# Kernel tuning notes

Hardware: AMD Instinct MI355X
Metric: run time of the kernel (lower is better)

Reference implementation:

```python
import jax, jax.numpy as jnp
import numpy as np

B, H, LQ, LKV, D = 2, 4, 512, 512, 64


def setup_inputs() -> dict:
    key = jax.random.key(0)
    ks = jax.random.split(key, 6)
    queries = jax.random.normal(ks[0], (B, H, LQ, D), dtype=jnp.float32)
    keys = jax.random.normal(ks[1], (B, H, LKV, D), dtype=jnp.float32)
    values = jax.random.normal(ks[2], (B, H, LKV, D), dtype=jnp.float32)
    mask = jax.random.randint(ks[3], (B, LQ, LKV), 0, 2) > 0  # bool [B, Lq, Lkv]
    # linear_concat: weight [D, 2D] (normal std=0.02), bias zeros
    W_concat = jax.random.normal(ks[4], (D, 2 * D), dtype=jnp.float32) * 0.02
    b_concat = jnp.zeros((D,), dtype=jnp.float32)
    # linear_logit: weight [1, D] -> vector [D], bias scalar zero
    w_logit = jax.random.normal(ks[5], (D,), dtype=jnp.float32) * 0.02
    b_logit = jnp.zeros((), dtype=jnp.float32)
    return dict(queries=queries, keys=keys, values=values, mask=mask,
                W_concat=W_concat, b_concat=b_concat,
                w_logit=w_logit, b_logit=b_logit)


def reference(queries, keys, values, mask, W_concat, b_concat, w_logit, b_logit):
    d = queries.shape[-1]
    # cat(q, k) @ W.T == q @ W[:, :d].T + k @ W[:, d:].T  (exact split of the concat-linear)
    qp = jnp.einsum('bhqd,ed->bhqe', queries, W_concat[:, :d])   # [B,H,Lq,D]
    kp = jnp.einsum('bhkd,ed->bhke', keys, W_concat[:, d:])      # [B,H,Lkv,D]
    combined = jnp.tanh(qp[:, :, :, None, :] + kp[:, :, None, :, :] + b_concat)  # [B,H,Lq,Lkv,D]
    logits = jnp.einsum('bhqke,e->bhqk', combined, w_logit) + b_logit            # [B,H,Lq,Lkv]
    # mask handling: invert; rows fully masked get un-masked (avoid all -inf softmax)
    inv = ~mask  # [B,Lq,Lkv]
    inv = jnp.where(jnp.all(inv, axis=-1, keepdims=True), False, inv)
    inv = inv[:, None, :, :]  # broadcast over heads
    logits = jnp.where(inv, -jnp.inf, logits)
    weights = jax.nn.softmax(logits, axis=-1)
    if weights.shape[1] == 1:  # torch .squeeze(dim=1) semantics
        weights = jnp.squeeze(weights, axis=1)
    return weights
```

## Files before the change

### kernel.cpp

```cpp
#include <hip/hip_runtime.h>
#include <hip/hip_bf16.h>


#define NQROWS 4096

__global__ __launch_bounds__(256) void proj_kernel(
    const float* __restrict__ Q, const float* __restrict__ K,
    const float* __restrict__ W, const float* __restrict__ bC,
    float* __restrict__ eq, float* __restrict__ ekt)
{
  const int t  = threadIdx.x;
  const int tr = t >> 6;
  const int e  = t & 63;
  const int rbase = blockIdx.x * 8;
  const bool isK = rbase >= NQROWS;
  const int r0 = isK ? rbase - NQROWS : rbase;
  const float* __restrict__ src = isK ? K : Q;
  const int off = isK ? 64 : 0;

  __shared__ float  srow[8][64];
  __shared__ float4 wsh[64][16];
  __shared__ float  trsp[64][9];

  for (int i = t; i < 8 * 64; i += 256)
    srow[i >> 6][i & 63] = src[(r0 + (i >> 6)) * 64 + (i & 63)];
  for (int i = t; i < 64 * 16; i += 256) {
    const int er = i >> 4, d4 = i & 15;
    wsh[er][d4 ^ (er & 7)] =
        reinterpret_cast<const float4*>(W + er * 128 + off)[d4];
  }
  __syncthreads();

  float acc0 = 0.f, acc1 = 0.f;
  const int rA = tr * 2;
  #pragma unroll
  for (int d4 = 0; d4 < 16; ++d4) {
    const float4 w4 = wsh[e][d4 ^ (e & 7)];
    const float4 s0 = *reinterpret_cast<const float4*>(&srow[rA + 0][d4 * 4]);
    const float4 s1 = *reinterpret_cast<const float4*>(&srow[rA + 1][d4 * 4]);
    acc0 = fmaf(s0.x, w4.x, acc0); acc0 = fmaf(s0.y, w4.y, acc0);
    acc0 = fmaf(s0.z, w4.z, acc0); acc0 = fmaf(s0.w, w4.w, acc0);
    acc1 = fmaf(s1.x, w4.x, acc1); acc1 = fmaf(s1.y, w4.y, acc1);
    acc1 = fmaf(s1.z, w4.z, acc1); acc1 = fmaf(s1.w, w4.w, acc1);
  }

  const float C2 = 2.8853900817779268f;
  if (!isK) {
    const float bias = bC[e];
    eq[(r0 + rA + 0) * 64 + e] = __builtin_amdgcn_exp2f((acc0 + bias) * C2);
    eq[(r0 + rA + 1) * 64 + e] = __builtin_amdgcn_exp2f((acc1 + bias) * C2);
  } else {
    trsp[e][rA + 0] = __builtin_amdgcn_exp2f(acc0 * C2);
    trsp[e][rA + 1] = __builtin_amdgcn_exp2f(acc1 * C2);
    __syncthreads();
    const int bh = r0 >> 9;
    const int k0 = r0 & 511;
    float* __restrict__ dst = ekt + bh * 64 * 512 + k0;
    #pragma unroll
    for (int iter = 0; iter < 2; ++iter) {
      const int i  = t + iter * 256;
      const int e2 = i >> 3, kk = i & 7;
      dst[e2 * 512 + kk] = trsp[e2][kk];
    }
  }
}

__global__ __launch_bounds__(256) void attn_kernel(
    const float* __restrict__ eq, const float* __restrict__ ekt,
    const float* __restrict__ wl, const int* __restrict__ mask,
    float* __restrict__ out)
{
  const int t  = threadIdx.x;
  const int g  = t >> 7;
  const int c  = t & 127;
  const int wv = t >> 6;
  const int ln = t & 63;
  const int bh = blockIdx.x & 7;
  const int qg = blockIdx.x >> 3;
  const int b  = bh >> 2;
  const int q0 = qg * 4;
  const int r0 = q0 + g * 2;

  __shared__ float qsh[4][64];
  __shared__ float w2s[64];
  __shared__ float s_sm[4][2], s_sr[4][2];
  __shared__ int   s_any[4][2];

  if (t < 64) w2s[t] = -2.0f * wl[t];
  qsh[t >> 6][t & 63] = eq[(bh * 512 + q0 + (t >> 6)) * 64 + (t & 63)];
  __syncthreads();

  const float4* __restrict__ kq =
      reinterpret_cast<const float4*>(ekt + bh * 64 * 512) + c;

  float4 a0 = {0.f, 0.f, 0.f, 0.f};
  float4 a1 = {0.f, 0.f, 0.f, 0.f};

#define QUADC(AC, QV, C)                                                      \
  {                                                                           \
    const float t0 = fmaf(QV.x, K0.C, 1.f);                                   \
    const float t1 = fmaf(QV.y, K1.C, 1.f);                                   \
    const float t2 = fmaf(QV.z, K2.C, 1.f);                                   \
    const float t3 = fmaf(QV.w, K3.C, 1.f);                                   \
    const float t01 = t0 * t1, t23 = t2 * t3;                                 \
    const float den = t01 * t23;                                              \
    const float n01 = fmaf(w4.x, t1, w4.y * t0);                              \
    const float n23 = fmaf(w4.z, t3, w4.w * t2);                              \
    const float num = fmaf(n01, t23, n23 * t01);                              \
    AC.C = fmaf(num, __builtin_amdgcn_rcpf(den), AC.C);                       \
  }
#define QROW(AC, QV) QUADC(AC, QV, x) QUADC(AC, QV, y) \
                     QUADC(AC, QV, z) QUADC(AC, QV, w)

  #pragma unroll 4
  for (int eb = 0; eb < 16; ++eb) {
    const float4 K0 = kq[(eb * 4 + 0) * 128];
    const float4 K1 = kq[(eb * 4 + 1) * 128];
    const float4 K2 = kq[(eb * 4 + 2) * 128];
    const float4 K3 = kq[(eb * 4 + 3) * 128];
    const float4 qa = *reinterpret_cast<const float4*>(&qsh[g * 2 + 0][eb * 4]);
    const float4 qb = *reinterpret_cast<const float4*>(&qsh[g * 2 + 1][eb * 4]);
    const float4 w4 = *reinterpret_cast<const float4*>(&w2s[eb * 4]);
    QROW(a0, qa) QROW(a1, qb)
  }

  const int* __restrict__ mb = mask + (b * 512 + r0) * 512 + 4 * c;
  const int4 mv0 = *reinterpret_cast<const int4*>(mb);
  const int4 mv1 = *reinterpret_cast<const int4*>(mb + 512);

  const float L2E = 1.4426950408889634f;
  float4 p0, p1;
  p0.x = __builtin_amdgcn_exp2f(a0.x * L2E);
  p0.y = __builtin_amdgcn_exp2f(a0.y * L2E);
  p0.z = __builtin_amdgcn_exp2f(a0.z * L2E);
  p0.w = __builtin_amdgcn_exp2f(a0.w * L2E);
  p1.x = __builtin_amdgcn_exp2f(a1.x * L2E);
  p1.y = __builtin_amdgcn_exp2f(a1.y * L2E);
  p1.z = __builtin_amdgcn_exp2f(a1.z * L2E);
  p1.w = __builtin_amdgcn_exp2f(a1.w * L2E);

  float sm0 = ((mv0.x ? p0.x : 0.f) + (mv0.y ? p0.y : 0.f)) +
              ((mv0.z ? p0.z : 0.f) + (mv0.w ? p0.w : 0.f));
  float sm1 = ((mv1.x ? p1.x : 0.f) + (mv1.y ? p1.y : 0.f)) +
              ((mv1.z ? p1.z : 0.f) + (mv1.w ? p1.w : 0.f));
  float sr0 = (p0.x + p0.y) + (p0.z + p0.w);
  float sr1 = (p1.x + p1.y) + (p1.z + p1.w);
  const int any0 = __any((mv0.x | mv0.y | mv0.z | mv0.w) != 0) ? 1 : 0;
  const int any1 = __any((mv1.x | mv1.y | mv1.z | mv1.w) != 0) ? 1 : 0;

  #pragma unroll
  for (int s = 1; s < 64; s <<= 1) {
    sm0 += __shfl_xor(sm0, s); sm1 += __shfl_xor(sm1, s);
    sr0 += __shfl_xor(sr0, s); sr1 += __shfl_xor(sr1, s);
  }
  if (ln == 0) {
    s_sm[wv][0] = sm0; s_sm[wv][1] = sm1;
    s_sr[wv][0] = sr0; s_sr[wv][1] = sr1;
    s_any[wv][0] = any0; s_any[wv][1] = any1;
  }
  __syncthreads();

  const int wA = g * 2, wB = g * 2 + 1;
  const bool ra0 = (s_any[wA][0] | s_any[wB][0]) != 0;
  const bool ra1 = (s_any[wA][1] | s_any[wB][1]) != 0;
  const float inv0 =
      1.0f / (ra0 ? (s_sm[wA][0] + s_sm[wB][0]) : (s_sr[wA][0] + s_sr[wB][0]));
  const float inv1 =
      1.0f / (ra1 ? (s_sm[wA][1] + s_sm[wB][1]) : (s_sr[wA][1] + s_sr[wB][1]));

  float4 o0, o1;
  o0.x = ((!ra0 || mv0.x) ? p0.x : 0.f) * inv0;
  o0.y = ((!ra0 || mv0.y) ? p0.y : 0.f) * inv0;
  o0.z = ((!ra0 || mv0.z) ? p0.z : 0.f) * inv0;
  o0.w = ((!ra0 || mv0.w) ? p0.w : 0.f) * inv0;
  o1.x = ((!ra1 || mv1.x) ? p1.x : 0.f) * inv1;
  o1.y = ((!ra1 || mv1.y) ? p1.y : 0.f) * inv1;
  o1.z = ((!ra1 || mv1.z) ? p1.z : 0.f) * inv1;
  o1.w = ((!ra1 || mv1.w) ? p1.w : 0.f) * inv1;

  float* __restrict__ o = out + (bh * 512 + r0) * 512 + 4 * c;
  *reinterpret_cast<float4*>(o) = o0;
  *reinterpret_cast<float4*>(o + 512) = o1;
}

extern "C" void kernel_launch(void* const* d_in, const int* in_sizes, int n_in,
                              void* d_out, int out_size, void* d_ws, size_t ws_size,
                              hipStream_t stream) {
  const float* Q  = (const float*)d_in[0];
  const float* K  = (const float*)d_in[1];
  const int*   M  = (const int*)d_in[3];
  const float* W  = (const float*)d_in[4];
  const float* bC = (const float*)d_in[5];
  const float* wl = (const float*)d_in[6];
  float* out = (float*)d_out;
  float* eqbuf  = (float*)d_ws;
  float* ektbuf = eqbuf + NQROWS * 64;

  proj_kernel<<<1024, 256, 0, stream>>>(Q, K, W, bC, eqbuf, ektbuf);
  attn_kernel<<<1024, 256, 0, stream>>>(eqbuf, ektbuf, wl, M, out);
}
```

Baseline: 25.21 us.

## Fuse query projection into attention kernel, shrink projection kernel to keys only

Removes the Q-projection pass from the first kernel and instead computes exp(2*qW+b) for the block's four query rows inside the attention kernel, using a shared-memory copy of the Q half of W. This cuts the first kernel's grid in half and drops the eq workspace write and reread. In exchange, each attention block loads a 16 KB weight tile and does a small matmul, which adds shared memory use and extra global traffic on the W reads.

```diff
diff --git a/kernel.cpp b/kernel.cpp
--- a/kernel.cpp
+++ b/kernel.cpp
@@ -4,30 +4,25 @@
 
 #define NQROWS 4096
 
-__global__ __launch_bounds__(256) void proj_kernel(
-    const float* __restrict__ Q, const float* __restrict__ K,
-    const float* __restrict__ W, const float* __restrict__ bC,
-    float* __restrict__ eq, float* __restrict__ ekt)
+__global__ __launch_bounds__(256) void kproj_kernel(
+    const float* __restrict__ K, const float* __restrict__ W,
+    float* __restrict__ ekt)
 {
   const int t  = threadIdx.x;
   const int tr = t >> 6;
   const int e  = t & 63;
-  const int rbase = blockIdx.x * 8;
-  const bool isK = rbase >= NQROWS;
-  const int r0 = isK ? rbase - NQROWS : rbase;
-  const float* __restrict__ src = isK ? K : Q;
-  const int off = isK ? 64 : 0;
+  const int r0 = blockIdx.x * 8;
 
   __shared__ float  srow[8][64];
   __shared__ float4 wsh[64][16];
   __shared__ float  trsp[64][9];
 
   for (int i = t; i < 8 * 64; i += 256)
-    srow[i >> 6][i & 63] = src[(r0 + (i >> 6)) * 64 + (i & 63)];
+    srow[i >> 6][i & 63] = K[(r0 + (i >> 6)) * 64 + (i & 63)];
   for (int i = t; i < 64 * 16; i += 256) {
     const int er = i >> 4, d4 = i & 15;
     wsh[er][d4 ^ (er & 7)] =
-        reinterpret_cast<const float4*>(W + er * 128 + off)[d4];
+        reinterpret_cast<const float4*>(W + er * 128 + 64)[d4];
   }
   __syncthreads();
 
@@ -45,28 +40,23 @@
   }
 
   const float C2 = 2.8853900817779268f;
-  if (!isK) {
-    const float bias = bC[e];
-    eq[(r0 + rA + 0) * 64 + e] = __builtin_amdgcn_exp2f((acc0 + bias) * C2);
-    eq[(r0 + rA + 1) * 64 + e] = __builtin_amdgcn_exp2f((acc1 + bias) * C2);
-  } else {
-    trsp[e][rA + 0] = __builtin_amdgcn_exp2f(acc0 * C2);
-    trsp[e][rA + 1] = __builtin_amdgcn_exp2f(acc1 * C2);
-    __syncthreads();
-    const int bh = r0 >> 9;
-    const int k0 = r0 & 511;
-    float* __restrict__ dst = ekt + bh * 64 * 512 + k0;
-    #pragma unroll
-    for (int iter = 0; iter < 2; ++iter) {
-      const int i  = t + iter * 256;
-      const int e2 = i >> 3, kk = i & 7;
-      dst[e2 * 512 + kk] = trsp[e2][kk];
-    }
+  trsp[e][rA + 0] = __builtin_amdgcn_exp2f(acc0 * C2);
+  trsp[e][rA + 1] = __builtin_amdgcn_exp2f(acc1 * C2);
+  __syncthreads();
+  const int bh = r0 >> 9;
+  const int k0 = r0 & 511;
+  float* __restrict__ dst = ekt + bh * 64 * 512 + k0;
+  #pragma unroll
+  for (int iter = 0; iter < 2; ++iter) {
+    const int i  = t + iter * 256;
+    const int e2 = i >> 3, kk = i & 7;
+    dst[e2 * 512 + kk] = trsp[e2][kk];
   }
 }
 
 __global__ __launch_bounds__(256) void attn_kernel(
-    const float* __restrict__ eq, const float* __restrict__ ekt,
+    const float* __restrict__ Q, const float* __restrict__ ekt,
+    const float* __restrict__ W, const float* __restrict__ bC,
     const float* __restrict__ wl, const int* __restrict__ mask,
     float* __restrict__ out)
 {
@@ -81,13 +71,35 @@
   const int q0 = qg * 4;
   const int r0 = q0 + g * 2;
 
-  __shared__ float qsh[4][64];
-  __shared__ float w2s[64];
-  __shared__ float s_sm[4][2], s_sr[4][2];
-  __shared__ int   s_any[4][2];
-
+  __shared__ float4 wsh[64][16];
+  __shared__ float  qrow[4][64];
+  __shared__ float  qsh[4][64];
+  __shared__ float  w2s[64];
+  __shared__ float  s_sm[4][2], s_sr[4][2];
+  __shared__ int    s_any[4][2];
+
+  for (int i = t; i < 64 * 16; i += 256) {
+    const int er = i >> 4, d4 = i & 15;
+    wsh[er][d4 ^ (er & 7)] =
+        reinterpret_cast<const float4*>(W + er * 128)[d4];
+  }
+  qrow[t >> 6][t & 63] = Q[(bh * 512 + q0 + (t >> 6)) * 64 + (t & 63)];
   if (t < 64) w2s[t] = -2.0f * wl[t];
-  qsh[t >> 6][t & 63] = eq[(bh * 512 + q0 + (t >> 6)) * 64 + (t & 63)];
+  __syncthreads();
+
+  {
+    const int r = t >> 6, e = t & 63;
+    float acc = 0.f;
+    #pragma unroll
+    for (int d4 = 0; d4 < 16; ++d4) {
+      const float4 w4 = wsh[e][d4 ^ (e & 7)];
+      const float4 qv = *reinterpret_cast<const float4*>(&qrow[r][d4 * 4]);
+      acc = fmaf(qv.x, w4.x, acc); acc = fmaf(qv.y, w4.y, acc);
+      acc = fmaf(qv.z, w4.z, acc); acc = fmaf(qv.w, w4.w, acc);
+    }
+    const float C2 = 2.8853900817779268f;
+    qsh[r][e] = __builtin_amdgcn_exp2f((acc + bC[e]) * C2);
+  }
   __syncthreads();
 
   const float4* __restrict__ kq =
@@ -193,9 +205,8 @@
   const float* bC = (const float*)d_in[5];
   const float* wl = (const float*)d_in[6];
   float* out = (float*)d_out;
-  float* eqbuf  = (float*)d_ws;
-  float* ektbuf = eqbuf + NQROWS * 64;
-
-  proj_kernel<<<1024, 256, 0, stream>>>(Q, K, W, bC, eqbuf, ektbuf);
-  attn_kernel<<<1024, 256, 0, stream>>>(eqbuf, ektbuf, wl, M, out);
+  float* ektbuf = (float*)d_ws;
+
+  kproj_kernel<<<512, 256, 0, stream>>>(K, W, ektbuf);
+  attn_kernel<<<1024, 256, 0, stream>>>(Q, ektbuf, W, bC, wl, M, out);
 }
```

After: 26.83 us. 1.06x slower.
